# Kernel optimization log

Hardware: AMD Instinct MI355X
Metric: run time of the kernel (lower is better)

## Reference

```python
import jax, jax.numpy as jnp
import numpy as np

EMBED_DIM = 128
NUM_HEADS = 16
D_K = EMBED_DIM // NUM_HEADS  # 8 qubits per head
DEPTH = 2

# Sign matrix for PauliZ expectations: wire w corresponds to bit (D_K-1-w) of the
# flattened state index (wire 0 = most significant axis, torchquantum convention).
_idx = np.arange(2 ** D_K)
_SIGNS = np.stack([1.0 - 2.0 * ((_idx >> (D_K - 1 - w)) & 1) for w in range(D_K)], axis=1).astype(np.float32)  # [2^d_k, d_k]


def quantum_layer(tokens, qparams):
    """Simulate the variational circuit for a batch of tokens.
    tokens: [N, d_k] real angles; qparams: [depth, d_k] trainable RX angles.
    RX(a)RX(b)=RX(a+b) on the same wire, so encoder + all depth RX layers
    compose into a single RX per wire. Then `depth` CNOT ladders, then <Z_w>.
    """
    theta = tokens + jnp.sum(qparams, axis=0)  # [N, d_k]
    half = 0.5 * theta
    # single-qubit amplitudes after RX(theta)|0>: [cos(t/2), -i sin(t/2)]
    amp = jnp.stack([jnp.cos(half).astype(jnp.complex64),
                     (-1j) * jnp.sin(half).astype(jnp.complex64)], axis=-1)  # [N, d_k, 2]
    # build product state [N, 2, 2, ..., 2]
    state = amp[:, 0, :]
    for i in range(1, D_K):
        state = jnp.einsum('n...,nq->n...q', state, amp[:, i, :])
    # depth x CNOT ladder: CNOT(i, i+1) for i in 0..d_k-2
    for _ in range(DEPTH):
        for i in range(D_K - 1):
            c_ax = 1 + i
            c0 = jnp.take(state, 0, axis=c_ax)
            c1 = jnp.take(state, 1, axis=c_ax)
            c1 = jnp.flip(c1, axis=c_ax)  # target axis = c_ax+1, shifted by -1 after take
            state = jnp.stack([c0, c1], axis=c_ax)
    probs = (state.real ** 2 + state.imag ** 2).reshape(state.shape[0], -1)  # [N, 2^d_k]
    return probs @ jnp.asarray(_SIGNS)  # [N, d_k]


def setup_inputs() -> dict:
    key = jax.random.key(0)
    ks = jax.random.split(key, 6)
    B, S, E = 4, 512, EMBED_DIM
    scale = 1.0 / np.sqrt(E)
    return {
        'x': jax.random.normal(ks[0], (B, S, E), dtype=jnp.float32),
        'Wq': jax.random.normal(ks[1], (E, E), dtype=jnp.float32) * scale,
        'Wk': jax.random.normal(ks[2], (E, E), dtype=jnp.float32) * scale,
        'Wv': jax.random.normal(ks[3], (E, E), dtype=jnp.float32) * scale,
        'Wo': jax.random.normal(ks[4], (E, E), dtype=jnp.float32) * scale,
        'qparams': jax.random.normal(ks[5], (DEPTH, D_K), dtype=jnp.float32),
    }


def reference(x, Wq, Wk, Wv, Wo, qparams):
    B, S, E = x.shape
    H, dk = NUM_HEADS, D_K
    # linear projections (torch Linear, no bias): y = x @ W.T
    q = (x @ Wq.T).reshape(B, S, H, dk).transpose(0, 2, 1, 3)  # [B,H,S,dk]
    k = (x @ Wk.T).reshape(B, S, H, dk).transpose(0, 2, 1, 3)
    v = (x @ Wv.T).reshape(B, S, H, dk).transpose(0, 2, 1, 3)
    # batched quantum circuit over all (batch, head, seq) tokens; shared weights
    qq = quantum_layer(q.reshape(-1, dk), qparams).reshape(B, H, S, dk)
    kq = quantum_layer(k.reshape(-1, dk), qparams).reshape(B, H, S, dk)
    vq = quantum_layer(v.reshape(-1, dk), qparams).reshape(B, H, S, dk)
    scores = jnp.einsum('bhqd,bhkd->bhqk', qq, kq) / jnp.sqrt(jnp.float32(dk))
    attn = jax.nn.softmax(scores, axis=-1)  # dropout in eval mode: identity
    out = jnp.einsum('bhqk,bhkd->bhqd', attn, vq)
    out = out.transpose(0, 2, 1, 3).reshape(B, S, E)
    return out @ Wo.T
```

## Files before the change

kernel.cpp:

```cpp
#include <hip/hip_runtime.h>
#include <cmath>

#define MATSZ 262144
#define QKV_OFF 0
#define AOUT_OFF (3 * MATSZ)

__global__ __launch_bounds__(256, 3) void k_qkvq(
    const float* __restrict__ x, const float* __restrict__ Wq,
    const float* __restrict__ Wk, const float* __restrict__ Wv,
    const float* __restrict__ qp, float* __restrict__ ws) {
  __shared__ float xs[8][128];
  __shared__ float th[2][8][128];
  const int t = threadIdx.x;
  const int tile = blockIdx.x;
  const int m = blockIdx.y;
  const float* W = (m == 0) ? Wq : (m == 1) ? Wk : Wv;
  const int e = t & 127, half = t >> 7;
  float4 w[16];
  {
    const float4* wr = (const float4*)W + (size_t)e * 32 + half * 16;
#pragma unroll
    for (int i = 0; i < 16; ++i) w[i] = wr[i];
  }
  ((float4*)&xs[0][0])[t] = ((const float4*)(x + (size_t)tile * 1024))[t];
  __syncthreads();
  const float4* xs4 = (const float4*)&xs[0][0];
#pragma unroll
  for (int r = 0; r < 8; ++r) {
    float a = 0.f;
    const float4* xr = xs4 + r * 32 + half * 16;
#pragma unroll
    for (int i = 0; i < 16; ++i) {
      float4 xv = xr[i];
      a = fmaf(xv.x, w[i].x, a);
      a = fmaf(xv.y, w[i].y, a);
      a = fmaf(xv.z, w[i].z, a);
      a = fmaf(xv.w, w[i].w, a);
    }
    th[half][r][e] = a;
  }
  __syncthreads();
  const int cg = t & 31, rg = t >> 5;
  const float4* th4 = (const float4*)&th[0][0][0];
  float4 s0 = th4[rg * 32 + cg];
  float4 s1 = th4[256 + rg * 32 + cg];
  float4 a4 = make_float4(s0.x + s1.x, s0.y + s1.y, s0.z + s1.z, s0.w + s1.w);
  const int j0 = (cg & 1) * 4;
  float4 qs;
  qs.x = qp[j0 + 0] + qp[8 + j0 + 0];
  qs.y = qp[j0 + 1] + qp[8 + j0 + 1];
  qs.z = qp[j0 + 2] + qp[8 + j0 + 2];
  qs.w = qp[j0 + 3] + qp[8 + j0 + 3];
  float4 c;
  c.x = __cosf(a4.x + qs.x);
  c.y = __cosf(a4.y + qs.y);
  c.z = __cosf(a4.z + qs.z);
  c.w = __cosf(a4.w + qs.w);
  float4 u;
  u.x = c.x; u.y = c.y; u.z = c.x * c.z; u.w = c.y * c.w;
  float gz = __shfl_xor(u.z, 1);
  float gw = __shfl_xor(u.w, 1);
  const bool hi = (cg & 1) != 0;
  float mz = hi ? gz : 1.f, mw = hi ? gw : 1.f;
  float4 o;
  o.x = u.x * mz; o.y = u.y * mw; o.z = u.z * mz; o.w = u.w * mw;
  const int h = cg >> 1;
  int row = tile * 8 + rg;
  int b = row >> 9, s = row & 511;
  float* dst = ws + QKV_OFF + (size_t)m * MATSZ +
               ((size_t)((b << 4) + h) * 512 + s) * 8 + (hi ? 4 : 0);
  *(float4*)dst = o;
}

__global__ __launch_bounds__(256, 4) void k_attn(
    float* __restrict__ ws) {
  __shared__ float4 kslo[512], kshi[512], vslo[512], vshi[512];
  const int qt = blockIdx.x;
  const int bh = blockIdx.y;
  const float* qkv = ws + QKV_OFF;
  const float* Qg = qkv + (size_t)bh * 4096;
  const float4* Kg = (const float4*)(qkv + MATSZ + (size_t)bh * 4096);
  const float4* Vg = (const float4*)(qkv + 2 * (size_t)MATSZ + (size_t)bh * 4096);
  const int t = threadIdx.x;
  for (int k = t; k < 512; k += 256) {
    kslo[k] = Kg[2 * k]; kshi[k] = Kg[2 * k + 1];
    vslo[k] = Vg[2 * k]; vshi[k] = Vg[2 * k + 1];
  }
  __syncthreads();
  const int qslot = t >> 4, ko = t & 15;
  const int row0 = qt * 32 + qslot * 2;
  const float scale = 0.51013389376f;
  float4 qa[2], qb[2];
#pragma unroll
  for (int r = 0; r < 2; ++r) {
    qa[r] = ((const float4*)(Qg + (size_t)(row0 + r) * 8))[0];
    qb[r] = ((const float4*)(Qg + (size_t)(row0 + r) * 8))[1];
    qa[r].x *= scale; qa[r].y *= scale; qa[r].z *= scale; qa[r].w *= scale;
    qb[r].x *= scale; qb[r].y *= scale; qb[r].z *= scale; qb[r].w *= scale;
  }
  float l[2] = {0.f, 0.f};
  float a[2][8];
#pragma unroll
  for (int r = 0; r < 2; ++r)
#pragma unroll
    for (int j = 0; j < 8; ++j) a[r][j] = 0.f;
#pragma unroll 4
  for (int i = 0; i < 32; ++i) {
    int k = i * 16 + ko;
    float4 kx = kslo[k], ky = kshi[k];
    float4 vx = vslo[k], vy = vshi[k];
#pragma unroll
    for (int r = 0; r < 2; ++r) {
      float s = qa[r].x * kx.x + qa[r].y * kx.y + qa[r].z * kx.z + qa[r].w * kx.w +
                qb[r].x * ky.x + qb[r].y * ky.y + qb[r].z * ky.z + qb[r].w * ky.w;
      float p = exp2f(s);
      l[r] += p;
      a[r][0] = fmaf(p, vx.x, a[r][0]);
      a[r][1] = fmaf(p, vx.y, a[r][1]);
      a[r][2] = fmaf(p, vx.z, a[r][2]);
      a[r][3] = fmaf(p, vx.w, a[r][3]);
      a[r][4] = fmaf(p, vy.x, a[r][4]);
      a[r][5] = fmaf(p, vy.y, a[r][5]);
      a[r][6] = fmaf(p, vy.z, a[r][6]);
      a[r][7] = fmaf(p, vy.w, a[r][7]);
    }
  }
#pragma unroll
  for (int mm = 1; mm <= 8; mm <<= 1) {
#pragma unroll
    for (int r = 0; r < 2; ++r) {
      l[r] += __shfl_xor(l[r], mm);
#pragma unroll
      for (int j = 0; j < 8; ++j) a[r][j] += __shfl_xor(a[r][j], mm);
    }
  }
  if (ko == 0) {
    int b = bh >> 4, h = bh & 15;
    float* aout = ws + AOUT_OFF;
#pragma unroll
    for (int r = 0; r < 2; ++r) {
      float inv = 1.f / l[r];
      float* d = aout + ((size_t)(b * 512 + row0 + r)) * 128 + h * 8;
      ((float4*)d)[0] = make_float4(a[r][0] * inv, a[r][1] * inv,
                                    a[r][2] * inv, a[r][3] * inv);
      ((float4*)d)[1] = make_float4(a[r][4] * inv, a[r][5] * inv,
                                    a[r][6] * inv, a[r][7] * inv);
    }
  }
}

__global__ __launch_bounds__(256, 2) void k_out(
    const float* __restrict__ ws, const float* __restrict__ Wo,
    float* __restrict__ out) {
  __shared__ float as_[4][128];
  __shared__ float th[2][4][128];
  const int t = threadIdx.x;
  const int tile = blockIdx.x;
  const float* aout = ws + AOUT_OFF;
  const int e = t & 127, half = t >> 7;
  float4 w[16];
  {
    const float4* wr = (const float4*)Wo + (size_t)e * 32 + half * 16;
#pragma unroll
    for (int i = 0; i < 16; ++i) w[i] = wr[i];
  }
  if (t < 128)
    ((float4*)&as_[0][0])[t] = ((const float4*)(aout + (size_t)tile * 512))[t];
  __syncthreads();
  const float4* as4 = (const float4*)&as_[0][0];
#pragma unroll
  for (int r = 0; r < 4; ++r) {
    float a = 0.f;
    const float4* ar = as4 + r * 32 + half * 16;
#pragma unroll
    for (int i = 0; i < 16; ++i) {
      float4 av = ar[i];
      a = fmaf(av.x, w[i].x, a);
      a = fmaf(av.y, w[i].y, a);
      a = fmaf(av.z, w[i].z, a);
      a = fmaf(av.w, w[i].w, a);
    }
    th[half][r][e] = a;
  }
  __syncthreads();
  if (t < 128) {
    const int cg = t & 31, rg = t >> 5;
    const float4* th4 = (const float4*)&th[0][0][0];
    float4 p0 = th4[rg * 32 + cg];
    float4 p1 = th4[128 + rg * 32 + cg];
    float4 o = make_float4(p0.x + p1.x, p0.y + p1.y, p0.z + p1.z, p0.w + p1.w);
    ((float4*)(out + (size_t)(tile * 4 + rg) * 128))[cg] = o;
  }
}

extern "C" void kernel_launch(void* const* d_in, const int* in_sizes, int n_in,
                              void* d_out, int out_size, void* d_ws, size_t ws_size,
                              hipStream_t stream) {
  const float* x  = (const float*)d_in[0];
  const float* Wq = (const float*)d_in[1];
  const float* Wk = (const float*)d_in[2];
  const float* Wv = (const float*)d_in[3];
  const float* Wo = (const float*)d_in[4];
  const float* qp = (const float*)d_in[5];
  float* out = (float*)d_out;
  float* ws = (float*)d_ws;

  hipLaunchKernelGGL(k_qkvq, dim3(256, 3), dim3(256), 0, stream,
                     x, Wq, Wk, Wv, qp, ws);
  hipLaunchKernelGGL(k_attn, dim3(16, 64), dim3(256), 0, stream, ws);
  hipLaunchKernelGGL(k_out, dim3(512), dim3(256), 0, stream, ws, Wo, out);
}
```

Measured before the change: 41.85 us.

## Fuse output projection into attention kernel via per-head atomic accumulation

Removes the separate output-projection kernel. Each attention block now keeps its 32x8 per-head result in shared memory and multiplies it by the matching 8-column slice of Wo, then adds the partial sums into the output with atomicAdd across the 16 heads. The output is zeroed inside the QKV kernel, and the softmax scale is folded into Q there. This saves one launch and the round trip of the attention output through global memory, at the cost of 16-way float atomic contention on every output element and nondeterministic summation order.

```diff
diff --git a/kernel.cpp b/kernel.cpp
--- a/kernel.cpp
+++ b/kernel.cpp
@@ -3,17 +3,21 @@
 
 #define MATSZ 262144
 #define QKV_OFF 0
-#define AOUT_OFF (3 * MATSZ)
 
 __global__ __launch_bounds__(256, 3) void k_qkvq(
     const float* __restrict__ x, const float* __restrict__ Wq,
     const float* __restrict__ Wk, const float* __restrict__ Wv,
-    const float* __restrict__ qp, float* __restrict__ ws) {
+    const float* __restrict__ qp, float* __restrict__ ws,
+    float* __restrict__ out) {
   __shared__ float xs[8][128];
   __shared__ float th[2][8][128];
   const int t = threadIdx.x;
   const int tile = blockIdx.x;
   const int m = blockIdx.y;
+  {
+    int gid = (m * 256 + tile) * 256 + t;
+    if (gid < 131072) ((float2*)out)[gid] = make_float2(0.f, 0.f);
+  }
   const float* W = (m == 0) ? Wq : (m == 1) ? Wk : Wv;
   const int e = t & 127, half = t >> 7;
   float4 w[16];
@@ -62,8 +66,10 @@
   float gw = __shfl_xor(u.w, 1);
   const bool hi = (cg & 1) != 0;
   float mz = hi ? gz : 1.f, mw = hi ? gw : 1.f;
+  const float osc = (m == 0) ? 0.51013389376f : 1.0f;
   float4 o;
-  o.x = u.x * mz; o.y = u.y * mw; o.z = u.z * mz; o.w = u.w * mw;
+  o.x = u.x * mz * osc; o.y = u.y * mw * osc;
+  o.z = u.z * mz * osc; o.w = u.w * mw * osc;
   const int h = cg >> 1;
   int row = tile * 8 + rg;
   int b = row >> 9, s = row & 511;
@@ -73,10 +79,13 @@
 }
 
 __global__ __launch_bounds__(256, 4) void k_attn(
-    float* __restrict__ ws) {
+    const float* __restrict__ ws, const float* __restrict__ Wo,
+    float* __restrict__ out) {
   __shared__ float4 kslo[512], kshi[512], vslo[512], vshi[512];
+  __shared__ float aout_s[32][8];
   const int qt = blockIdx.x;
   const int bh = blockIdx.y;
+  const int b = bh >> 4, h = bh & 15;
   const float* qkv = ws + QKV_OFF;
   const float* Qg = qkv + (size_t)bh * 4096;
   const float4* Kg = (const float4*)(qkv + MATSZ + (size_t)bh * 4096);
@@ -89,14 +98,11 @@
   __syncthreads();
   const int qslot = t >> 4, ko = t & 15;
   const int row0 = qt * 32 + qslot * 2;
-  const float scale = 0.51013389376f;
   float4 qa[2], qb[2];
 #pragma unroll
   for (int r = 0; r < 2; ++r) {
     qa[r] = ((const float4*)(Qg + (size_t)(row0 + r) * 8))[0];
     qb[r] = ((const float4*)(Qg + (size_t)(row0 + r) * 8))[1];
-    qa[r].x *= scale; qa[r].y *= scale; qa[r].z *= scale; qa[r].w *= scale;
-    qb[r].x *= scale; qb[r].y *= scale; qb[r].z *= scale; qb[r].w *= scale;
   }
   float l[2] = {0.f, 0.f};
   float a[2][8];
@@ -111,8 +117,9 @@
     float4 vx = vslo[k], vy = vshi[k];
 #pragma unroll
     for (int r = 0; r < 2; ++r) {
-      float s = qa[r].x * kx.x + qa[r].y * kx.y + qa[r].z * kx.z + qa[r].w * kx.w +
-                qb[r].x * ky.x + qb[r].y * ky.y + qb[r].z * ky.z + qb[r].w * ky.w;
+      float s = qa[r].x * kx.x + qa[r].y * kx.y + qa[r].z * kx.z +
+                qa[r].w * kx.w + qb[r].x * ky.x + qb[r].y * ky.y +
+                qb[r].z * ky.z + qb[r].w * ky.w;
       float p = exp2f(s);
       l[r] += p;
       a[r][0] = fmaf(p, vx.x, a[r][0]);
@@ -135,61 +142,26 @@
     }
   }
   if (ko == 0) {
-    int b = bh >> 4, h = bh & 15;
-    float* aout = ws + AOUT_OFF;
 #pragma unroll
     for (int r = 0; r < 2; ++r) {
       float inv = 1.f / l[r];
-      float* d = aout + ((size_t)(b * 512 + row0 + r)) * 128 + h * 8;
+      float* d = &aout_s[qslot * 2 + r][0];
       ((float4*)d)[0] = make_float4(a[r][0] * inv, a[r][1] * inv,
                                     a[r][2] * inv, a[r][3] * inv);
       ((float4*)d)[1] = make_float4(a[r][4] * inv, a[r][5] * inv,
                                     a[r][6] * inv, a[r][7] * inv);
     }
   }
-}
-
-__global__ __launch_bounds__(256, 2) void k_out(
-    const float* __restrict__ ws, const float* __restrict__ Wo,
-    float* __restrict__ out) {
-  __shared__ float as_[4][128];
-  __shared__ float th[2][4][128];
-  const int t = threadIdx.x;
-  const int tile = blockIdx.x;
-  const float* aout = ws + AOUT_OFF;
-  const int e = t & 127, half = t >> 7;
-  float4 w[16];
-  {
-    const float4* wr = (const float4*)Wo + (size_t)e * 32 + half * 16;
-#pragma unroll
-    for (int i = 0; i < 16; ++i) w[i] = wr[i];
-  }
-  if (t < 128)
-    ((float4*)&as_[0][0])[t] = ((const float4*)(aout + (size_t)tile * 512))[t];
   __syncthreads();
-  const float4* as4 = (const float4*)&as_[0][0];
-#pragma unroll
-  for (int r = 0; r < 4; ++r) {
-    float a = 0.f;
-    const float4* ar = as4 + r * 32 + half * 16;
-#pragma unroll
-    for (int i = 0; i < 16; ++i) {
-      float4 av = ar[i];
-      a = fmaf(av.x, w[i].x, a);
-      a = fmaf(av.y, w[i].y, a);
-      a = fmaf(av.z, w[i].z, a);
-      a = fmaf(av.w, w[i].w, a);
-    }
-    th[half][r][e] = a;
-  }
-  __syncthreads();
-  if (t < 128) {
-    const int cg = t & 31, rg = t >> 5;
-    const float4* th4 = (const float4*)&th[0][0][0];
-    float4 p0 = th4[rg * 32 + cg];
-    float4 p1 = th4[128 + rg * 32 + cg];
-    float4 o = make_float4(p0.x + p1.x, p0.y + p1.y, p0.z + p1.z, p0.w + p1.w);
-    ((float4*)(out + (size_t)(tile * 4 + rg) * 128))[cg] = o;
+  const int e = t >> 1, jh = (t & 1) * 4;
+  const float4 wv = *(const float4*)(Wo + (size_t)e * 128 + h * 8 + jh);
+  float* obase = out + ((size_t)(b * 512 + qt * 32)) * 128 + e;
+#pragma unroll 4
+  for (int row = 0; row < 32; ++row) {
+    const float4 av = *(const float4*)&aout_s[row][jh];
+    float p = av.x * wv.x + av.y * wv.y + av.z * wv.z + av.w * wv.w;
+    p += __shfl_xor(p, 1);
+    if ((t & 1) == 0) atomicAdd(obase + (size_t)row * 128, p);
   }
 }
 
@@ -206,7 +178,7 @@
   float* ws = (float*)d_ws;
 
   hipLaunchKernelGGL(k_qkvq, dim3(256, 3), dim3(256), 0, stream,
-                     x, Wq, Wk, Wv, qp, ws);
-  hipLaunchKernelGGL(k_attn, dim3(16, 64), dim3(256), 0, stream, ws);
-  hipLaunchKernelGGL(k_out, dim3(512), dim3(256), 0, stream, ws, Wo, out);
+                     x, Wq, Wk, Wv, qp, ws, out);
+  hipLaunchKernelGGL(k_attn, dim3(16, 64), dim3(256), 0, stream,
+                     ws, Wo, out);
 }
```

Measured after the change: 43.10 us. 1.03x slower.
